# Performance work log

Hardware: AMD Instinct MI355X
Metric: run time of the kernel (lower is better)

## Reference

```python
import jax, jax.numpy as jnp
import numpy as np

B = 4
N1_PER = 16384  # fine points per scene
N2_PER = 4096   # coarse points per scene
IN_PLANES = 512
OUT_PLANES = 256
K = 3
CHUNK = 2048
BN_EPS = 1e-5


def _bn(x, g, b, m, v):
    # eval-mode BatchNorm1d: affine normalize with running stats
    return (x - m) * (g / jnp.sqrt(v + BN_EPS)) + b


def _interpolate_one(p1b, p2b, f2b):
    # p1b: [n1,3] queries, p2b: [n2,3] support, f2b: [n2,C]
    # k=3 inverse-distance weighted interpolation (pointops.interpolation)
    pq = p1b.reshape(-1, CHUNK, 3)  # chunk queries to avoid full [n1,n2] matrix

    def step(carry, q):  # q: [CHUNK,3]
        d2 = jnp.sum((q[:, None, :] - p2b[None, :, :]) ** 2, axis=-1)  # [CHUNK,n2]
        neg_d2, idx = jax.lax.top_k(-d2, K)                            # [CHUNK,K]
        dist = jnp.sqrt(jnp.maximum(-neg_d2, 1e-12))
        w = 1.0 / (dist + 1e-8)
        w = w / jnp.sum(w, axis=-1, keepdims=True)
        feat = f2b[idx]  # [CHUNK,K,C] gather
        return carry, jnp.einsum('qk,qkc->qc', w, feat)

    _, out = jax.lax.scan(step, None, pq)
    return out.reshape(-1, f2b.shape[-1])  # [n1,C]


def _forward(p1, x1, p2, x2, W1, b1, g1, be1, m1, v1, W2, b2, g2, be2, m2, v2):
    # branch 1: Linear-BN-ReLU on fine features
    h1 = jax.nn.relu(_bn(x1 @ W1.T + b1, g1, be1, m1, v1))  # [N1, out]
    # branch 2: Linear-BN-ReLU on coarse features, then kNN interpolation up
    h2 = jax.nn.relu(_bn(x2 @ W2.T + b2, g2, be2, m2, v2))  # [N2, out]
    # equal-sized scenes -> reshape + vmap over batch (offsets are [n,2n,...])
    p1b = p1.reshape(B, N1_PER, 3)
    p2b = p2.reshape(B, N2_PER, 3)
    h2b = h2.reshape(B, N2_PER, -1)
    up = jax.vmap(_interpolate_one)(p1b, p2b, h2b).reshape(-1, h2.shape[-1])
    return h1 + up


def setup_inputs() -> dict:
    key = jax.random.key(0)
    ks = jax.random.split(key, 16)
    p1 = jax.random.normal(ks[0], (B * N1_PER, 3), dtype=jnp.float32)
    x1 = jax.random.normal(ks[1], (B * N1_PER, OUT_PLANES), dtype=jnp.float32)
    p2 = jax.random.normal(ks[2], (B * N2_PER, 3), dtype=jnp.float32)
    x2 = jax.random.normal(ks[3], (B * N2_PER, IN_PLANES), dtype=jnp.float32)
    o1 = (jnp.arange(1, B + 1) * N1_PER).astype(jnp.int64)
    o2 = (jnp.arange(1, B + 1) * N2_PER).astype(jnp.int64)
    s1 = 1.0 / np.sqrt(OUT_PLANES)
    s2 = 1.0 / np.sqrt(IN_PLANES)
    W1 = jax.random.uniform(ks[4], (OUT_PLANES, OUT_PLANES), minval=-s1, maxval=s1)
    b1 = jax.random.uniform(ks[5], (OUT_PLANES,), minval=-s1, maxval=s1)
    W2 = jax.random.uniform(ks[6], (OUT_PLANES, IN_PLANES), minval=-s2, maxval=s2)
    b2 = jax.random.uniform(ks[7], (OUT_PLANES,), minval=-s2, maxval=s2)
    g1 = jnp.ones((OUT_PLANES,)); be1 = jnp.zeros((OUT_PLANES,))
    m1 = 0.1 * jax.random.normal(ks[8], (OUT_PLANES,))
    v1 = jax.random.uniform(ks[9], (OUT_PLANES,), minval=0.5, maxval=1.5)
    g2 = jnp.ones((OUT_PLANES,)); be2 = jnp.zeros((OUT_PLANES,))
    m2 = 0.1 * jax.random.normal(ks[10], (OUT_PLANES,))
    v2 = jax.random.uniform(ks[11], (OUT_PLANES,), minval=0.5, maxval=1.5)
    return dict(p1=p1, x1=x1, p2=p2, x2=x2, W1=W1, b1=b1, g1=g1, be1=be1,
                m1=m1, v1=v1, W2=W2, b2=b2, g2=g2, be2=be2, m2=m2, v2=v2,
                o1=o1, o2=o2)


def reference(p1, x1, p2, x2, W1, b1, g1, be1, m1, v1, W2, b2, g2, be2, m2, v2, o1, o2):
    return _forward(p1, x1, p2, x2, W1, b1, g1, be1, m1, v1, W2, b2, g2, be2, m2, v2)
```

## Files before the change

### kernel.cpp

```cpp
#include <hip/hip_runtime.h>

#define BM 128
#define BNT 128
#define BK 32
#define LDK 40

typedef __bf16 bf16x8 __attribute__((ext_vector_type(8)));
typedef float  f32x4  __attribute__((ext_vector_type(4)));
typedef float  f32x2  __attribute__((ext_vector_type(2)));

static __device__ __forceinline__ unsigned short f2bf(float f) {
  union { float f; unsigned int i; } c; c.f = f;
  unsigned int u = c.i;
  u += 0x7FFFu + ((u >> 16) & 1u);
  return (unsigned short)(u >> 16);
}

static __device__ __forceinline__ uint4 pk8(const float4 a, const float4 b) {
  uint4 o;
  o.x = ((unsigned int)f2bf(a.y) << 16) | f2bf(a.x);
  o.y = ((unsigned int)f2bf(a.w) << 16) | f2bf(a.z);
  o.z = ((unsigned int)f2bf(b.y) << 16) | f2bf(b.x);
  o.w = ((unsigned int)f2bf(b.w) << 16) | f2bf(b.z);
  return o;
}

#define WSEG0 65536u
#define WSEG1 196608u

__global__ __launch_bounds__(256) void cvt_w(const float* __restrict__ s0,
                                             const float* __restrict__ s1,
                                             unsigned short* __restrict__ dst) {
  const unsigned int e = (blockIdx.x * 256u + threadIdx.x) * 8u;
  const float* sp; unsigned int off;
  if (e < WSEG0) { sp = s0; off = e; }
  else           { sp = s1; off = e - WSEG0; }
  const float4* p = (const float4*)(sp + off);
  *(uint4*)(dst + e) = pk8(p[0], p[1]);
}

template<bool FUSE>
__global__ __launch_bounds__(256) void gemm_bn_relu_k(
    const float* __restrict__ A,
    const unsigned short* __restrict__ Wm,
    const float* __restrict__ bias,
    const float* __restrict__ gam,
    const float* __restrict__ bet,
    const float* __restrict__ rmean,
    const float* __restrict__ rvar,
    const int K,
    float* __restrict__ outp,
    const float* __restrict__ h2f,
    const float* __restrict__ wgt,
    const int* __restrict__ idxg)
{
  __shared__ unsigned short As[BM][LDK];
  __shared__ unsigned short Bs[BNT][LDK];
  __shared__ float SC[BNT];
  __shared__ float SH[BNT];
  __shared__ float Wt[BM * 3];
  __shared__ int   Id[BM * 3];

  const int tid = threadIdx.x;
  const int bm = blockIdx.x, bn = blockIdx.y;

  if (tid < BNT) {
    const int ch = bn * BNT + tid;
    const float sc = gam[ch] / sqrtf(rvar[ch] + 1e-5f);
    SC[tid] = sc;
    SH[tid] = (bias[ch] - rmean[ch]) * sc + bet[ch];
  }
  if (FUSE) {
    for (int i = tid; i < BM * 3; i += 256) {
      Wt[i] = wgt[bm * (BM * 3) + i];
      Id[i] = idxg[bm * (BM * 3) + i];
    }
  }

  const int wave = tid >> 6, lane = tid & 63;
  const int wr = (wave >> 1) * 64, wc = (wave & 1) * 64;
  const int lr = lane & 15;
  const int kq = (lane >> 4) * 8;

  const int r0 = tid >> 2, co = (tid & 3) * 8;
  const int r1 = 64 + r0;
  const float* Ar0 = A + (size_t)(bm * BM + r0) * K + co;
  const float* Ar1 = A + (size_t)(bm * BM + r1) * K + co;
  const unsigned short* Br0 = Wm + (size_t)(bn * BNT + r0) * K + co;
  const unsigned short* Br1 = Wm + (size_t)(bn * BNT + r1) * K + co;

  f32x4 acc[4][4];
  const f32x4 zero = {0.f, 0.f, 0.f, 0.f};
#pragma unroll
  for (int i = 0; i < 4; ++i)
#pragma unroll
    for (int j = 0; j < 4; ++j) acc[i][j] = zero;

  float4 fa00 = *(const float4*)(Ar0);
  float4 fa01 = *(const float4*)(Ar0 + 4);
  float4 fa10 = *(const float4*)(Ar1);
  float4 fa11 = *(const float4*)(Ar1 + 4);
  uint4 vb0 = *(const uint4*)(Br0);
  uint4 vb1 = *(const uint4*)(Br1);

  for (int k0 = 0; k0 < K; k0 += BK) {
    __syncthreads();
    *(uint4*)&As[r0][co] = pk8(fa00, fa01);
    *(uint4*)&As[r1][co] = pk8(fa10, fa11);
    *(uint4*)&Bs[r0][co] = vb0;
    *(uint4*)&Bs[r1][co] = vb1;
    __syncthreads();
    if (k0 + BK < K) {
      fa00 = *(const float4*)(Ar0 + k0 + BK);
      fa01 = *(const float4*)(Ar0 + k0 + BK + 4);
      fa10 = *(const float4*)(Ar1 + k0 + BK);
      fa11 = *(const float4*)(Ar1 + k0 + BK + 4);
      vb0 = *(const uint4*)(Br0 + k0 + BK);
      vb1 = *(const uint4*)(Br1 + k0 + BK);
    }
    bf16x8 af[4], bv[4];
#pragma unroll
    for (int mi = 0; mi < 4; ++mi)
      af[mi] = *(const bf16x8*)&As[wr + mi * 16 + lr][kq];
#pragma unroll
    for (int ni = 0; ni < 4; ++ni)
      bv[ni] = *(const bf16x8*)&Bs[wc + ni * 16 + lr][kq];
#pragma unroll
    for (int mi = 0; mi < 4; ++mi)
#pragma unroll
      for (int ni = 0; ni < 4; ++ni)
        acc[mi][ni] = __builtin_amdgcn_mfma_f32_16x16x32_bf16(af[mi], bv[ni], acc[mi][ni], 0, 0, 0);
  }

#pragma unroll
  for (int mi = 0; mi < 4; ++mi) {
#pragma unroll
    for (int r = 0; r < 4; ++r) {
      const int rloc = wr + mi * 16 + (lane >> 4) * 4 + r;
      const size_t grow = (size_t)(bm * BM + rloc);
      float w0 = 0.f, w1 = 0.f, w2 = 0.f;
      const float *g0 = nullptr, *g1 = nullptr, *g2 = nullptr;
      if (FUSE) {
        w0 = Wt[rloc * 3 + 0]; w1 = Wt[rloc * 3 + 1]; w2 = Wt[rloc * 3 + 2];
        g0 = h2f + (size_t)Id[rloc * 3 + 0] * 256;
        g1 = h2f + (size_t)Id[rloc * 3 + 1] * 256;
        g2 = h2f + (size_t)Id[rloc * 3 + 2] * 256;
      }
#pragma unroll
      for (int ni = 0; ni < 4; ++ni) {
        const int cloc = wc + ni * 16 + lr;
        const int gcol = bn * BNT + cloc;
        float v = acc[mi][ni][r] * SC[cloc] + SH[cloc];
        v = fmaxf(v, 0.f);
        if (FUSE) v += w0 * g0[gcol] + w1 * g1[gcol] + w2 * g2[gcol];
        outp[grow * 256 + gcol] = v;
      }
    }
  }
}

__global__ __launch_bounds__(256) void prep_pairs(const float* __restrict__ p2,
                                                  float* __restrict__ pp) {
  const int m = blockIdx.x * 256 + threadIdx.x;
  const float* s = p2 + m * 6;
  float* d = pp + m * 8;
  d[0] = s[0]; d[1] = s[3];
  d[2] = s[1]; d[3] = s[4];
  d[4] = s[2]; d[5] = s[5];
  d[6] = 0.f;  d[7] = 0.f;
}

__global__ __launch_bounds__(256) void knn_partial(const float* __restrict__ p1,
                                                   const float* __restrict__ ppair,
                                                   float* __restrict__ s_part,
                                                   int* __restrict__ i_part) {
#pragma clang fp contract(off)
  const int tid = threadIdx.x;
  const int qb = blockIdx.x, sp = blockIdx.y;
  const int scene = qb >> 6;
  const int pbase = scene * 4096 + sp * 1024;
  const int qi = qb * 256 + tid;

  const float qx = p1[qi * 3 + 0];
  const float qy = p1[qi * 3 + 1];
  const float qz = p1[qi * 3 + 2];
  const f32x2 qxx = {qx, qx}, qyy = {qy, qy}, qzz = {qz, qz};

  float s0 = 1e30f, s1 = 1e30f, s2 = 1e30f;
  int i0 = pbase, i1 = pbase, i2 = pbase;

  const f32x2* pp = (const f32x2*)(ppair + (size_t)(pbase >> 1) * 8);
#pragma unroll 4
  for (int m = 0; m < 512; ++m) {
    const f32x2 X = pp[m * 4 + 0];
    const f32x2 Y = pp[m * 4 + 1];
    const f32x2 Z = pp[m * 4 + 2];
    const f32x2 dx = qxx - X;
    const f32x2 dy = qyy - Y;
    const f32x2 dz = qzz - Z;
    const f32x2 sv = (dx * dx + dy * dy) + dz * dz;
    const int jg = pbase + 2 * m;
    const float sa = sv.x, sb = sv.y;
    if (sa < s2) {
      if (sa < s1) {
        s2 = s1; i2 = i1;
        if (sa < s0) { s1 = s0; i1 = i0; s0 = sa; i0 = jg; }
        else         { s1 = sa; i1 = jg; }
      } else { s2 = sa; i2 = jg; }
    }
    if (sb < s2) {
      if (sb < s1) {
        s2 = s1; i2 = i1;
        if (sb < s0) { s1 = s0; i1 = i0; s0 = sb; i0 = jg + 1; }
        else         { s1 = sb; i1 = jg + 1; }
      } else { s2 = sb; i2 = jg + 1; }
    }
  }
  const int ob = (qi * 4 + sp) * 3;
  s_part[ob + 0] = s0; s_part[ob + 1] = s1; s_part[ob + 2] = s2;
  i_part[ob + 0] = i0; i_part[ob + 1] = i1; i_part[ob + 2] = i2;
}

__global__ __launch_bounds__(256) void knn_merge(const float* __restrict__ s_part,
                                                 const int* __restrict__ i_part,
                                                 float* __restrict__ wgt,
                                                 int* __restrict__ idxg) {
  const int qi = blockIdx.x * 256 + threadIdx.x;

  float s0 = 1e30f, s1 = 1e30f, s2 = 1e30f;
  int i0 = 0, i1 = 0, i2 = 0;
  const int base = qi * 12;
#pragma unroll
  for (int t = 0; t < 12; ++t) {
    const float s = s_part[base + t];
    const int id = i_part[base + t];
    if (s < s2) {
      if (s < s1) {
        s2 = s1; i2 = i1;
        if (s < s0) { s1 = s0; i1 = i0; s0 = s; i0 = id; }
        else        { s1 = s;  i1 = id; }
      } else { s2 = s; i2 = id; }
    }
  }
  const float d0 = sqrtf(fmaxf(s0, 1e-12f));
  const float d1 = sqrtf(fmaxf(s1, 1e-12f));
  const float d2 = sqrtf(fmaxf(s2, 1e-12f));
  float w0 = 1.f / (d0 + 1e-8f);
  float w1 = 1.f / (d1 + 1e-8f);
  float w2 = 1.f / (d2 + 1e-8f);
  const float inv = 1.f / (w0 + w1 + w2);
  wgt[qi * 3 + 0] = w0 * inv; wgt[qi * 3 + 1] = w1 * inv; wgt[qi * 3 + 2] = w2 * inv;
  idxg[qi * 3 + 0] = i0; idxg[qi * 3 + 1] = i1; idxg[qi * 3 + 2] = i2;
}

extern "C" void kernel_launch(void* const* d_in, const int* in_sizes, int n_in,
                              void* d_out, int out_size, void* d_ws, size_t ws_size,
                              hipStream_t stream) {
  const float* p1 = (const float*)d_in[0];
  const float* x1 = (const float*)d_in[1];
  const float* p2 = (const float*)d_in[2];
  const float* x2 = (const float*)d_in[3];
  const float* W1 = (const float*)d_in[4];
  const float* b1 = (const float*)d_in[5];
  const float* g1 = (const float*)d_in[6];
  const float* be1 = (const float*)d_in[7];
  const float* m1 = (const float*)d_in[8];
  const float* v1 = (const float*)d_in[9];
  const float* W2 = (const float*)d_in[10];
  const float* b2 = (const float*)d_in[11];
  const float* g2 = (const float*)d_in[12];
  const float* be2 = (const float*)d_in[13];
  const float* m2 = (const float*)d_in[14];
  const float* v2 = (const float*)d_in[15];

  char* ws = (char*)d_ws;
  unsigned short* W1b = (unsigned short*)ws;
  unsigned short* W2b = (unsigned short*)(ws + 131072);
  float* s_part = (float*)(ws + 1048576);
  int*   i_part = (int*)(ws + 4194304);
  float* h2f    = (float*)(ws + 8388608);
  float* ppair  = (float*)(ws + 25165824);
  float* wgt    = (float*)(ws + 25427968);
  int*   idxg   = (int*)(ws + 26214400);

  float* outp = (float*)d_out;

  cvt_w<<<96, 256, 0, stream>>>(W1, W2, W1b);

  gemm_bn_relu_k<false><<<dim3(128, 2), 256, 0, stream>>>(
      x2, W2b, b2, g2, be2, m2, v2, 512, h2f, nullptr, nullptr, nullptr);

  prep_pairs<<<32, 256, 0, stream>>>(p2, ppair);

  knn_partial<<<dim3(256, 4), 256, 0, stream>>>(p1, ppair, s_part, i_part);

  knn_merge<<<256, 256, 0, stream>>>(s_part, i_part, wgt, idxg);

  gemm_bn_relu_k<true><<<dim3(512, 2), 256, 0, stream>>>(
      x1, W1b, b1, g1, be1, m1, v1, 256, outp, h2f, wgt, idxg);
}
```

Measured before the change: 347.4 us.

## Stage whole weight slice in LDS, stream A from global, split kNN support 8 ways

The GEMM kernels now load the block's full 128-row weight slice into LDS once. Each wave reads its A rows straight from global memory into registers as bf16, so the per-k-step LDS staging and double barriers go away. Separately, the kNN partial search splits each scene's support set into 8 parts of 512 points instead of 4, which doubles the grid for more parallelism at the cost of a larger merge and a bigger partial buffer. A fragments now come from uncoalesced per-lane global loads, and the LDS footprint grows with K, which may lower occupancy.

```diff
diff --git a/kernel.cpp b/kernel.cpp
--- a/kernel.cpp
+++ b/kernel.cpp
@@ -1,9 +1,4 @@
 #include <hip/hip_runtime.h>
-
-#define BM 128
-#define BNT 128
-#define BK 32
-#define LDK 40
 
 typedef __bf16 bf16x8 __attribute__((ext_vector_type(8)));
 typedef float  f32x4  __attribute__((ext_vector_type(4)));
@@ -23,6 +18,12 @@
   o.z = ((unsigned int)f2bf(b.y) << 16) | f2bf(b.x);
   o.w = ((unsigned int)f2bf(b.w) << 16) | f2bf(b.z);
   return o;
+}
+
+static __device__ __forceinline__ bf16x8 pk8bf(const float4 a, const float4 b) {
+  uint4 u = pk8(a, b);
+  union { uint4 u; bf16x8 v; } c; c.u = u;
+  return c.v;
 }
 
 #define WSEG0 65536u
@@ -39,8 +40,8 @@
   *(uint4*)(dst + e) = pk8(p[0], p[1]);
 }
 
-template<bool FUSE>
-__global__ __launch_bounds__(256) void gemm_bn_relu_k(
+template<int K, bool FUSE>
+__global__ __launch_bounds__(256) void gemm_wlds_k(
     const float* __restrict__ A,
     const unsigned short* __restrict__ Wm,
     const float* __restrict__ bias,
@@ -48,96 +49,76 @@
     const float* __restrict__ bet,
     const float* __restrict__ rmean,
     const float* __restrict__ rvar,
-    const int K,
     float* __restrict__ outp,
     const float* __restrict__ h2f,
     const float* __restrict__ wgt,
     const int* __restrict__ idxg)
 {
-  __shared__ unsigned short As[BM][LDK];
-  __shared__ unsigned short Bs[BNT][LDK];
-  __shared__ float SC[BNT];
-  __shared__ float SH[BNT];
-  __shared__ float Wt[BM * 3];
-  __shared__ int   Id[BM * 3];
+  constexpr int LDW = K + 8;
+  __shared__ unsigned short WL[128][LDW];
+  __shared__ float SC[128];
+  __shared__ float SH[128];
+  __shared__ float Wt[FUSE ? 128 * 3 : 1];
+  __shared__ int   Id[FUSE ? 128 * 3 : 1];
 
   const int tid = threadIdx.x;
-  const int bm = blockIdx.x, bn = blockIdx.y;
-
-  if (tid < BNT) {
-    const int ch = bn * BNT + tid;
+  const int bn = blockIdx.x;
+  const int by = blockIdx.y;
+
+  constexpr int CH = K / 8;
+  for (int i = tid; i < 128 * CH; i += 256) {
+    const int r = i / CH, c = (i % CH) * 8;
+    *(uint4*)&WL[r][c] = *(const uint4*)(Wm + (size_t)(bn * 128 + r) * K + c);
+  }
+  if (tid < 128) {
+    const int ch = bn * 128 + tid;
     const float sc = gam[ch] / sqrtf(rvar[ch] + 1e-5f);
     SC[tid] = sc;
     SH[tid] = (bias[ch] - rmean[ch]) * sc + bet[ch];
   }
   if (FUSE) {
-    for (int i = tid; i < BM * 3; i += 256) {
-      Wt[i] = wgt[bm * (BM * 3) + i];
-      Id[i] = idxg[bm * (BM * 3) + i];
-    }
-  }
+    for (int i = tid; i < 128 * 3; i += 256) {
+      Wt[i] = wgt[by * (128 * 3) + i];
+      Id[i] = idxg[by * (128 * 3) + i];
+    }
+  }
+  __syncthreads();
 
   const int wave = tid >> 6, lane = tid & 63;
-  const int wr = (wave >> 1) * 64, wc = (wave & 1) * 64;
   const int lr = lane & 15;
   const int kq = (lane >> 4) * 8;
-
-  const int r0 = tid >> 2, co = (tid & 3) * 8;
-  const int r1 = 64 + r0;
-  const float* Ar0 = A + (size_t)(bm * BM + r0) * K + co;
-  const float* Ar1 = A + (size_t)(bm * BM + r1) * K + co;
-  const unsigned short* Br0 = Wm + (size_t)(bn * BNT + r0) * K + co;
-  const unsigned short* Br1 = Wm + (size_t)(bn * BNT + r1) * K + co;
-
-  f32x4 acc[4][4];
+  const int row0 = by * 128 + wave * 32;
+
+  const float* Ap0 = A + (size_t)(row0 + lr) * K + kq;
+  const float* Ap1 = A + (size_t)(row0 + 16 + lr) * K + kq;
+
+  f32x4 acc[2][8];
   const f32x4 zero = {0.f, 0.f, 0.f, 0.f};
 #pragma unroll
-  for (int i = 0; i < 4; ++i)
-#pragma unroll
-    for (int j = 0; j < 4; ++j) acc[i][j] = zero;
-
-  float4 fa00 = *(const float4*)(Ar0);
-  float4 fa01 = *(const float4*)(Ar0 + 4);
-  float4 fa10 = *(const float4*)(Ar1);
-  float4 fa11 = *(const float4*)(Ar1 + 4);
-  uint4 vb0 = *(const uint4*)(Br0);
-  uint4 vb1 = *(const uint4*)(Br1);
-
-  for (int k0 = 0; k0 < K; k0 += BK) {
-    __syncthreads();
-    *(uint4*)&As[r0][co] = pk8(fa00, fa01);
-    *(uint4*)&As[r1][co] = pk8(fa10, fa11);
-    *(uint4*)&Bs[r0][co] = vb0;
-    *(uint4*)&Bs[r1][co] = vb1;
-    __syncthreads();
-    if (k0 + BK < K) {
-      fa00 = *(const float4*)(Ar0 + k0 + BK);
-      fa01 = *(const float4*)(Ar0 + k0 + BK + 4);
-      fa10 = *(const float4*)(Ar1 + k0 + BK);
-      fa11 = *(const float4*)(Ar1 + k0 + BK + 4);
-      vb0 = *(const uint4*)(Br0 + k0 + BK);
-      vb1 = *(const uint4*)(Br1 + k0 + BK);
-    }
-    bf16x8 af[4], bv[4];
-#pragma unroll
-    for (int mi = 0; mi < 4; ++mi)
-      af[mi] = *(const bf16x8*)&As[wr + mi * 16 + lr][kq];
-#pragma unroll
-    for (int ni = 0; ni < 4; ++ni)
-      bv[ni] = *(const bf16x8*)&Bs[wc + ni * 16 + lr][kq];
-#pragma unroll
-    for (int mi = 0; mi < 4; ++mi)
-#pragma unroll
-      for (int ni = 0; ni < 4; ++ni)
-        acc[mi][ni] = __builtin_amdgcn_mfma_f32_16x16x32_bf16(af[mi], bv[ni], acc[mi][ni], 0, 0, 0);
-  }
-
-#pragma unroll
-  for (int mi = 0; mi < 4; ++mi) {
+  for (int mi = 0; mi < 2; ++mi)
+#pragma unroll
+    for (int ni = 0; ni < 8; ++ni) acc[mi][ni] = zero;
+
+#pragma unroll 4
+  for (int kk = 0; kk < K; kk += 32) {
+    const bf16x8 a0 = pk8bf(*(const float4*)(Ap0 + kk),
+                            *(const float4*)(Ap0 + kk + 4));
+    const bf16x8 a1 = pk8bf(*(const float4*)(Ap1 + kk),
+                            *(const float4*)(Ap1 + kk + 4));
+#pragma unroll
+    for (int ni = 0; ni < 8; ++ni) {
+      const bf16x8 bv = *(const bf16x8*)&WL[ni * 16 + lr][kk + kq];
+      acc[0][ni] = __builtin_amdgcn_mfma_f32_16x16x32_bf16(a0, bv, acc[0][ni], 0, 0, 0);
+      acc[1][ni] = __builtin_amdgcn_mfma_f32_16x16x32_bf16(a1, bv, acc[1][ni], 0, 0, 0);
+    }
+  }
+
+#pragma unroll
+  for (int mi = 0; mi < 2; ++mi) {
 #pragma unroll
     for (int r = 0; r < 4; ++r) {
-      const int rloc = wr + mi * 16 + (lane >> 4) * 4 + r;
-      const size_t grow = (size_t)(bm * BM + rloc);
+      const int rloc = wave * 32 + mi * 16 + (lane >> 4) * 4 + r;
+      const size_t grow = (size_t)(by * 128 + rloc);
       float w0 = 0.f, w1 = 0.f, w2 = 0.f;
       const float *g0 = nullptr, *g1 = nullptr, *g2 = nullptr;
       if (FUSE) {
@@ -147,9 +128,9 @@
         g2 = h2f + (size_t)Id[rloc * 3 + 2] * 256;
       }
 #pragma unroll
-      for (int ni = 0; ni < 4; ++ni) {
-        const int cloc = wc + ni * 16 + lr;
-        const int gcol = bn * BNT + cloc;
+      for (int ni = 0; ni < 8; ++ni) {
+        const int cloc = ni * 16 + lr;
+        const int gcol = bn * 128 + cloc;
         float v = acc[mi][ni][r] * SC[cloc] + SH[cloc];
         v = fmaxf(v, 0.f);
         if (FUSE) v += w0 * g0[gcol] + w1 * g1[gcol] + w2 * g2[gcol];
@@ -178,7 +159,7 @@
   const int tid = threadIdx.x;
   const int qb = blockIdx.x, sp = blockIdx.y;
   const int scene = qb >> 6;
-  const int pbase = scene * 4096 + sp * 1024;
+  const int pbase = scene * 4096 + sp * 512;
   const int qi = qb * 256 + tid;
 
   const float qx = p1[qi * 3 + 0];
@@ -191,7 +172,7 @@
 
   const f32x2* pp = (const f32x2*)(ppair + (size_t)(pbase >> 1) * 8);
 #pragma unroll 4
-  for (int m = 0; m < 512; ++m) {
+  for (int m = 0; m < 256; ++m) {
     const f32x2 X = pp[m * 4 + 0];
     const f32x2 Y = pp[m * 4 + 1];
     const f32x2 Z = pp[m * 4 + 2];
@@ -216,7 +197,7 @@
       } else { s2 = sb; i2 = jg + 1; }
     }
   }
-  const int ob = (qi * 4 + sp) * 3;
+  const int ob = (qi * 8 + sp) * 3;
   s_part[ob + 0] = s0; s_part[ob + 1] = s1; s_part[ob + 2] = s2;
   i_part[ob + 0] = i0; i_part[ob + 1] = i1; i_part[ob + 2] = i2;
 }
@@ -229,9 +210,9 @@
 
   float s0 = 1e30f, s1 = 1e30f, s2 = 1e30f;
   int i0 = 0, i1 = 0, i2 = 0;
-  const int base = qi * 12;
-#pragma unroll
-  for (int t = 0; t < 12; ++t) {
+  const int base = qi * 24;
+#pragma unroll
+  for (int t = 0; t < 24; ++t) {
     const float s = s_part[base + t];
     const int id = i_part[base + t];
     if (s < s2) {
@@ -277,25 +258,25 @@
   unsigned short* W1b = (unsigned short*)ws;
   unsigned short* W2b = (unsigned short*)(ws + 131072);
   float* s_part = (float*)(ws + 1048576);
-  int*   i_part = (int*)(ws + 4194304);
-  float* h2f    = (float*)(ws + 8388608);
-  float* ppair  = (float*)(ws + 25165824);
-  float* wgt    = (float*)(ws + 25427968);
-  int*   idxg   = (int*)(ws + 26214400);
+  int*   i_part = (int*)(ws + 7340032);
+  float* h2f    = (float*)(ws + 16777216);
+  float* ppair  = (float*)(ws + 33554432);
+  float* wgt    = (float*)(ws + 33816576);
+  int*   idxg   = (int*)(ws + 34603008);
 
   float* outp = (float*)d_out;
 
   cvt_w<<<96, 256, 0, stream>>>(W1, W2, W1b);
 
-  gemm_bn_relu_k<false><<<dim3(128, 2), 256, 0, stream>>>(
-      x2, W2b, b2, g2, be2, m2, v2, 512, h2f, nullptr, nullptr, nullptr);
+  gemm_wlds_k<512, false><<<dim3(2, 128), 256, 0, stream>>>(
+      x2, W2b, b2, g2, be2, m2, v2, h2f, nullptr, nullptr, nullptr);
 
   prep_pairs<<<32, 256, 0, stream>>>(p2, ppair);
 
-  knn_partial<<<dim3(256, 4), 256, 0, stream>>>(p1, ppair, s_part, i_part);
+  knn_partial<<<dim3(256, 8), 256, 0, stream>>>(p1, ppair, s_part, i_part);
 
   knn_merge<<<256, 256, 0, stream>>>(s_part, i_part, wgt, idxg);
 
-  gemm_bn_relu_k<true><<<dim3(512, 2), 256, 0, stream>>>(
-      x1, W1b, b1, g1, be1, m1, v1, 256, outp, h2f, wgt, idxg);
-}
+  gemm_wlds_k<256, true><<<dim3(2, 512), 256, 0, stream>>>(
+      x1, W1b, b1, g1, be1, m1, v1, outp, h2f, wgt, idxg);
+}
```

Result: slower. 383.6 us (+10.4%).
